# Performance work log

Hardware: AMD Instinct MI355X
Metric: run time of the kernel (lower is better)

Reference implementation:

```python
import jax, jax.numpy as jnp
import numpy as np

EPS = 1e-5  # torch GroupNorm default eps


def gn(x, g, b):
    # GroupNorm with 1 group on [N, C]: normalize over channel dim per row
    mu = jnp.mean(x, axis=-1, keepdims=True)
    var = jnp.var(x, axis=-1, keepdims=True)
    return (x - mu) * jax.lax.rsqrt(var + EPS) * g + b


def setup_inputs() -> dict:
    N, A, E, D = 500000, 20000, 500000, 128
    key = jax.random.key(0)
    ks = jax.random.split(key, 12)
    s = 0.05
    return {
        "map_x": jax.random.normal(ks[0], (N, 8), jnp.float32),
        "agt_x": jax.random.normal(ks[1], (A, 80), jnp.float32),
        "u": jax.random.randint(ks[2], (E,), 0, A),
        "v": jax.random.randint(ks[3], (E,), 0, N),
        # map_fc: Linear(8,D) with bias, then custom Linear(D,D,bias=False)+GN+ReLU
        "W0": jax.random.normal(ks[4], (D, 8), jnp.float32) * s,
        "b0": jnp.zeros((D,), jnp.float32),
        "W1": jax.random.normal(ks[5], (D, D), jnp.float32) * s,
        "g1": jnp.ones((D,), jnp.float32),
        "b1": jnp.zeros((D,), jnp.float32),
        # agt_fc: Linear(80, D, bias=False)
        "Wa": jax.random.normal(ks[6], (D, 80), jnp.float32) * s,
        # self.bn GroupNorm params
        "g_bn": jnp.ones((D,), jnp.float32),
        "b_bn": jnp.zeros((D,), jnp.float32),
        # self.fc: Linear(2D, D, bias=False)+GN+ReLU
        "Wf": jax.random.normal(ks[7], (D, 2 * D), jnp.float32) * s,
        "g_fc": jnp.ones((D,), jnp.float32),
        "b_fc": jnp.zeros((D,), jnp.float32),
    }


def reference(map_x, agt_x, u, v, W0, b0, W1, g1, b1, Wa, g_bn, b_bn, Wf, g_fc, b_fc):
    # map_fc: Linear+ReLU, then Linear(no bias)+GN+ReLU
    h = jax.nn.relu(map_x @ W0.T + b0)                      # [N, D]
    h = jax.nn.relu(gn(h @ W1.T, g1, b1))                   # [N, D]
    # agent messages: project agents once (A < E), then gather per edge
    msg = (agt_x @ Wa.T)[u]                                 # [E, D]
    tmp = jnp.zeros_like(h).at[v].add(msg)                  # scatter-add into map nodes
    tmp = jax.nn.relu(gn(tmp, g_bn, b_bn))                  # [N, D]
    cat = jnp.concatenate([h, tmp], axis=-1)                # [N, 2D]
    out = jax.nn.relu(gn(cat @ Wf.T, g_fc, b_fc))           # [N, D]
    return out
```

## Files before the change

### kernel.cpp

```cpp
#include <hip/hip_runtime.h>
#include <stdint.h>

#define EPS 1e-5f

typedef short bh8 __attribute__((ext_vector_type(8)));
typedef float f4v __attribute__((ext_vector_type(4)));
typedef unsigned short ushort_t;

static __device__ __forceinline__ unsigned short f2bf(float f) {
    unsigned u = __builtin_bit_cast(unsigned, f);
    u += 0x7fffu + ((u >> 16) & 1u);
    return (unsigned short)(u >> 16);
}

static __device__ __forceinline__ float bfbits(unsigned x) {
    return __builtin_bit_cast(float, x);
}

static __device__ __forceinline__ void acc16(float* tv, uint4 qa, uint4 qb) {
    unsigned wd[8] = {qa.x, qa.y, qa.z, qa.w, qb.x, qb.y, qb.z, qb.w};
#pragma unroll
    for (int p = 0; p < 8; ++p) {
        tv[2 * p + 0] += bfbits(wd[p] << 16);
        tv[2 * p + 1] += bfbits(wd[p] & 0xffff0000u);
    }
}


__global__ void prep(const float* __restrict__ W1, const float* __restrict__ Wf,
                     const float* __restrict__ Wa, ushort_t* __restrict__ W1b,
                     ushort_t* __restrict__ Wfb, float* __restrict__ WaT) {
    int i = blockIdx.x * 256 + threadIdx.x;
    if (i < 16384) W1b[i] = f2bf(W1[i]);
    else if (i < 49152) { int j = i - 16384; Wfb[j] = f2bf(Wf[j]); }
    else if (i < 59392) { int l2 = i - 49152; int k = l2 >> 7, c = l2 & 127; WaT[l2] = Wa[c * 80 + k]; }
}

__global__ __launch_bounds__(256) void proj_agents(const float* __restrict__ agt,
                                                   const float* __restrict__ WaT,
                                                   unsigned short* __restrict__ Pb) {
    __shared__ float WT[80 * 128];
    __shared__ float xT[80][32];
    int t = threadIdx.x;
    int row0 = blockIdx.x * 32;
#pragma unroll
    for (int m = 0; m < 40; ++m) WT[t + 256 * m] = WaT[t + 256 * m];
#pragma unroll
    for (int m = 0; m < 10; ++m) {
        int f = t + 256 * m;
        int r = f / 80, k = f - r * 80;
        xT[k][r] = agt[(size_t)(row0 + r) * 80 + k];
    }
    __syncthreads();
    int tx = t & 31, ty = t >> 5;
    float acc[4][4] = {};
    for (int k = 0; k < 80; ++k) {
        float4 xv = *(const float4*)&xT[k][ty * 4];
        float4 wv = *(const float4*)&WT[k * 128 + tx * 4];
        float xa[4] = {xv.x, xv.y, xv.z, xv.w};
        float wa[4] = {wv.x, wv.y, wv.z, wv.w};
#pragma unroll
        for (int i = 0; i < 4; ++i)
#pragma unroll
            for (int j = 0; j < 4; ++j) acc[i][j] = fmaf(xa[i], wa[j], acc[i][j]);
    }
#pragma unroll
    for (int i = 0; i < 4; ++i) {
        int r = row0 + ty * 4 + i;
        union { unsigned short s[4]; uint2 q; } o;
#pragma unroll
        for (int j = 0; j < 4; ++j) o.s[j] = f2bf(acc[i][j]);
        *(uint2*)&Pb[(size_t)r * 128 + tx * 4] = o.q;
    }
}

__global__ void hist_v(const int* __restrict__ v, int* __restrict__ cnt, int E) {
    int e = blockIdx.x * 256 + threadIdx.x;
    if (e < E) atomicAdd(&cnt[v[e]], 1);
}

__global__ __launch_bounds__(256) void scan1(const int* __restrict__ cnt,
                                             int* __restrict__ rp,
                                             int* __restrict__ partials, int n) {
    __shared__ int lds[256];
    int b = blockIdx.x, t = threadIdx.x;
    int base = b * 4096 + t * 16;
    int vv[16];
    int run = 0;
#pragma unroll
    for (int i = 0; i < 16; ++i) {
        int c = (base + i < n) ? cnt[base + i] : 0;
        vv[i] = run;
        run += c;
    }
    lds[t] = run;
    __syncthreads();
#pragma unroll
    for (int off = 1; off < 256; off <<= 1) {
        int x = (t >= off) ? lds[t - off] : 0;
        __syncthreads();
        lds[t] += x;
        __syncthreads();
    }
    int excl = lds[t] - run;
    if (t == 255) partials[b] = lds[255];
#pragma unroll
    for (int i = 0; i < 16; ++i)
        if (base + i < n) rp[base + i] = excl + vv[i];
}

__global__ __launch_bounds__(256) void scan2(int* __restrict__ partials, int nb) {
    __shared__ int lds[256];
    int t = threadIdx.x;
    int vv = (t < nb) ? partials[t] : 0;
    lds[t] = vv;
    __syncthreads();
#pragma unroll
    for (int off = 1; off < 256; off <<= 1) {
        int x = (t >= off) ? lds[t - off] : 0;
        __syncthreads();
        lds[t] += x;
        __syncthreads();
    }
    if (t < nb) partials[t] = lds[t] - vv;
}

__global__ void scan3(int* __restrict__ rp, const int* __restrict__ partials,
                      int n, int E) {
    int i = blockIdx.x * 256 + threadIdx.x;
    if (i < n) rp[i] += partials[i >> 12];
    if (i == 0) rp[n] = E;
}

__global__ void fill_csr(const int* __restrict__ u, const int* __restrict__ v,
                         const int* __restrict__ rp, int* __restrict__ cursor,
                         int* __restrict__ col, int E) {
    int e = blockIdx.x * 256 + threadIdx.x;
    if (e < E) {
        int vv = v[e];
        int pos = rp[vv] + atomicAdd(&cursor[vv], 1);
        col[pos] = u[e];
    }
}

__global__ __launch_bounds__(256) void gather_gn(
    const unsigned short* __restrict__ Pb, const int* __restrict__ rp,
    const int* __restrict__ col, const float* __restrict__ g_bn,
    const float* __restrict__ b_bn, ushort_t* __restrict__ catB) {
    const int t = threadIdx.x;
    const int node = blockIdx.x * 32 + (t >> 3);
    const int c0 = (t & 7) * 16;
    const int beg = rp[node];
    const int deg = rp[node + 1] - beg;
    const int ca = col[(deg > 0) ? beg : 0];
    const int cb = col[(deg > 1) ? beg + 1 : 0];
    const int cc = col[(deg > 2) ? beg + 2 : 0];
    const int cd = col[(deg > 3) ? beg + 3 : 0];
    const unsigned short* pB = Pb + c0;
    float tv[16] = {};
    if (deg > 0) { const uint4* p = (const uint4*)(pB + (size_t)ca * 128); acc16(tv, p[0], p[1]); }
    if (deg > 1) { const uint4* p = (const uint4*)(pB + (size_t)cb * 128); acc16(tv, p[0], p[1]); }
    if (deg > 2) { const uint4* p = (const uint4*)(pB + (size_t)cc * 128); acc16(tv, p[0], p[1]); }
    if (deg > 3) { const uint4* p = (const uint4*)(pB + (size_t)cd * 128); acc16(tv, p[0], p[1]); }
    for (int k = 4; k < deg; ++k) {
        const uint4* p = (const uint4*)(pB + (size_t)col[beg + k] * 128);
        acc16(tv, p[0], p[1]);
    }
    float a = 0.f, q = 0.f;
#pragma unroll
    for (int i = 0; i < 16; ++i) { a += tv[i]; q += tv[i] * tv[i]; }
#pragma unroll
    for (int msk = 1; msk < 8; msk <<= 1) {
        a += __shfl_xor(a, msk, 64);
        q += __shfl_xor(q, msk, 64);
    }
    const float mean = a * (1.f / 128.f);
    const float var = q * (1.f / 128.f) - mean * mean;
    const float inv = rsqrtf(var + EPS);
    union { unsigned short s[16]; uint4 q4[2]; } o;
#pragma unroll
    for (int i = 0; i < 16; ++i) {
        const int cch = c0 + i;
        o.s[i] = f2bf(fmaxf((tv[i] - mean) * inv * g_bn[cch] + b_bn[cch], 0.f));
    }
    uint4* dst = (uint4*)(catB + (size_t)node * 128 + c0);
    dst[0] = o.q4[0];
    dst[1] = o.q4[1];
}

__global__ __launch_bounds__(512, 4) void fused(
    const float* __restrict__ mapx, const float* __restrict__ W0,
    const float* __restrict__ b0, const ushort_t* __restrict__ W1b,
    const float* __restrict__ g1, const float* __restrict__ b1,
    const ushort_t* __restrict__ catB, const ushort_t* __restrict__ Wfb,
    const float* __restrict__ g_fc, const float* __restrict__ b_fc,
    float* __restrict__ out, int ntiles)
{
    __shared__ __align__(16) short h0s[32 * 128];
    __shared__ __align__(16) short cats[32 * 256];
    __shared__ float W0s[128 * 8];
    __shared__ float b0s[128];
    __shared__ float2 part[8][32];
    __shared__ float gA[128], bA[128], gC[128], bC[128];

    const int t = threadIdx.x;
    const int w = t >> 6;
    const int l = t & 63;
    const int l15 = l & 15, lg = l >> 4;

    if (t < 128) {
        gA[t] = g1[t];   bA[t] = b1[t];
        gC[t] = g_fc[t]; bC[t] = b_fc[t];
        b0s[t] = b0[t];
    }
    for (int i = t; i < 1024; i += 512) W0s[i] = W0[i];

    bh8 w1b[4], wfb[8];
    {
        const int wr = 16 * w + l15;
#pragma unroll
        for (int s = 0; s < 4; ++s)
            w1b[s] = *(const bh8*)(W1b + (size_t)wr * 128 + s * 32 + lg * 8);
#pragma unroll
        for (int s = 0; s < 8; ++s)
            wfb[s] = *(const bh8*)(Wfb + (size_t)wr * 256 + s * 32 + lg * 8);
    }
    __syncthreads();

    const f4v fzero = {0.f, 0.f, 0.f, 0.f};
    const int stride = (int)gridDim.x;

    for (int tile = blockIdx.x; tile < ntiles; tile += stride) {
        const int row0 = tile * 32;

        {
            const int r = t & 31, cg = t >> 5;
            float mx[8];
            const float* p = mapx + (size_t)(row0 + r) * 8;
            *(float4*)&mx[0] = *(const float4*)p;
            *(float4*)&mx[4] = *(const float4*)(p + 4);
            __align__(16) unsigned short hb[8];
#pragma unroll
            for (int c = 0; c < 8; ++c) {
                const int cc = 8 * cg + c;
                float a = b0s[cc];
#pragma unroll
                for (int j = 0; j < 8; ++j) a = fmaf(mx[j], W0s[cc * 8 + j], a);
                hb[c] = f2bf(fmaxf(a, 0.f));
            }
            const int a = (r * 256 + cg * 16) ^ ((r & 7) << 4);
            *(uint4*)((char*)h0s + a) = *(const uint4*)&hb[0];
        }
        {
            const int r2 = t >> 4, cb = (t & 15) * 8;
            uint4 q = *(const uint4*)(catB + (size_t)(row0 + r2) * 128 + cb);
            const int ad = (r2 * 512 + 256 + cb * 2) ^ ((r2 & 7) << 4);
            *(uint4*)((char*)cats + ad) = q;
        }
        __syncthreads();

        f4v acc2[2];
        acc2[0] = fzero; acc2[1] = fzero;
#pragma unroll
        for (int s = 0; s < 4; ++s) {
            bh8 af[2];
#pragma unroll
            for (int m = 0; m < 2; ++m) {
                const int row = 16 * m + l15;
                const int a = (row * 256 + s * 64 + lg * 16) ^ ((row & 7) << 4);
                af[m] = *(const bh8*)((const char*)h0s + a);
            }
#pragma unroll
            for (int m = 0; m < 2; ++m)
                acc2[m] = __builtin_amdgcn_mfma_f32_16x16x32_bf16(
                    w1b[s], af[m], acc2[m], 0, 0, 0);
        }

#pragma unroll
        for (int m = 0; m < 2; ++m) {
            float a = acc2[m][0] + acc2[m][1] + acc2[m][2] + acc2[m][3];
            float q = acc2[m][0] * acc2[m][0] + acc2[m][1] * acc2[m][1] +
                      acc2[m][2] * acc2[m][2] + acc2[m][3] * acc2[m][3];
            a += __shfl_xor(a, 16, 64); q += __shfl_xor(q, 16, 64);
            a += __shfl_xor(a, 32, 64); q += __shfl_xor(q, 32, 64);
            if (lg == 0) part[w][16 * m + l15] = make_float2(a, q);
        }
        __syncthreads();

#pragma unroll
        for (int m = 0; m < 2; ++m) {
            const int row = 16 * m + l15;
            float a = 0.f, q = 0.f;
#pragma unroll
            for (int pw = 0; pw < 8; ++pw) {
                float2 pq = part[pw][row];
                a += pq.x; q += pq.y;
            }
            const float mean = a * (1.f / 128.f);
            const float var = q * (1.f / 128.f) - mean * mean;
            const float inv = rsqrtf(var + EPS);
            const int c00 = 16 * w + 4 * lg;
            union { unsigned short s[4]; uint2 q2; } o;
#pragma unroll
            for (int reg = 0; reg < 4; ++reg) {
                float v2 = (acc2[m][reg] - mean) * inv * gA[c00 + reg] + bA[c00 + reg];
                o.s[reg] = f2bf(fmaxf(v2, 0.f));
            }
            const int ad = (row * 512 + c00 * 2) ^ ((row & 7) << 4);
            *(uint2*)((char*)cats + ad) = o.q2;
        }
        __syncthreads();

        f4v acc3[2];
        acc3[0] = fzero; acc3[1] = fzero;
#pragma unroll
        for (int s = 0; s < 8; ++s) {
            bh8 af[2];
#pragma unroll
            for (int m = 0; m < 2; ++m) {
                const int row = 16 * m + l15;
                const int a = (row * 512 + s * 64 + lg * 16) ^ ((row & 7) << 4);
                af[m] = *(const bh8*)((const char*)cats + a);
            }
#pragma unroll
            for (int m = 0; m < 2; ++m)
                acc3[m] = __builtin_amdgcn_mfma_f32_16x16x32_bf16(
                    wfb[s], af[m], acc3[m], 0, 0, 0);
        }

#pragma unroll
        for (int m = 0; m < 2; ++m) {
            float a = acc3[m][0] + acc3[m][1] + acc3[m][2] + acc3[m][3];
            float q = acc3[m][0] * acc3[m][0] + acc3[m][1] * acc3[m][1] +
                      acc3[m][2] * acc3[m][2] + acc3[m][3] * acc3[m][3];
            a += __shfl_xor(a, 16, 64); q += __shfl_xor(q, 16, 64);
            a += __shfl_xor(a, 32, 64); q += __shfl_xor(q, 32, 64);
            if (lg == 0) part[w][16 * m + l15] = make_float2(a, q);
        }
        __syncthreads();

#pragma unroll
        for (int m = 0; m < 2; ++m) {
            const int row = 16 * m + l15;
            float a = 0.f, q = 0.f;
#pragma unroll
            for (int pw = 0; pw < 8; ++pw) {
                float2 pq = part[pw][row];
                a += pq.x; q += pq.y;
            }
            const float mean = a * (1.f / 128.f);
            const float var = q * (1.f / 128.f) - mean * mean;
            const float inv = rsqrtf(var + EPS);
            const int c00 = 16 * w + 4 * lg;
            float4 o;
            o.x = fmaxf((acc3[m][0] - mean) * inv * gC[c00 + 0] + bC[c00 + 0], 0.f);
            o.y = fmaxf((acc3[m][1] - mean) * inv * gC[c00 + 1] + bC[c00 + 1], 0.f);
            o.z = fmaxf((acc3[m][2] - mean) * inv * gC[c00 + 2] + bC[c00 + 2], 0.f);
            o.w = fmaxf((acc3[m][3] - mean) * inv * gC[c00 + 3] + bC[c00 + 3], 0.f);
            *(float4*)&out[(size_t)(row0 + row) * 128 + c00] = o;
        }
        __syncthreads();
    }
}

extern "C" void kernel_launch(void* const* d_in, const int* in_sizes, int n_in,
                              void* d_out, int out_size, void* d_ws, size_t ws_size,
                              hipStream_t stream) {
    const float* mapx = (const float*)d_in[0];
    const float* agt  = (const float*)d_in[1];
    const int*   u    = (const int*)d_in[2];
    const int*   v    = (const int*)d_in[3];
    const float* W0   = (const float*)d_in[4];
    const float* b0   = (const float*)d_in[5];
    const float* W1   = (const float*)d_in[6];
    const float* g1   = (const float*)d_in[7];
    const float* b1   = (const float*)d_in[8];
    const float* Wa   = (const float*)d_in[9];
    const float* g_bn = (const float*)d_in[10];
    const float* b_bn = (const float*)d_in[11];
    const float* Wf   = (const float*)d_in[12];
    const float* g_fc = (const float*)d_in[13];
    const float* b_fc = (const float*)d_in[14];
    int N = in_sizes[0] / 8;
    int A = in_sizes[1] / 80;
    int E = in_sizes[2];
    float* out = (float*)d_out;

    char* ws = (char*)d_ws;
    unsigned short* Pb  = (unsigned short*)(ws + 0);
    float*    WaT       = (float*)(ws + 5120000);
    ushort_t* W1b       = (ushort_t*)(ws + 5160960);
    ushort_t* Wfb       = (ushort_t*)(ws + 5193728);
    int*      cnt       = (int*)(ws + 5259264);
    int*      cursor    = (int*)(ws + 7259264);
    int*      rp        = (int*)(ws + 9259264);
    int*      partials  = (int*)(ws + 11259392);
    int*      colv      = (int*)(ws + 11261440);
    ushort_t* catB      = (ushort_t*)(ws + 16777216);

    const int nb_scan = (N + 4095) / 4096;
    const int nb_e = (E + 255) / 256;

    prep<<<232, 256, 0, stream>>>(W1, Wf, Wa, W1b, Wfb, WaT);
    hipMemsetAsync(cnt, 0, 4000000, stream);
    hist_v<<<nb_e, 256, 0, stream>>>(v, cnt, E);
    proj_agents<<<A / 32, 256, 0, stream>>>(agt, WaT, Pb);
    scan1<<<nb_scan, 256, 0, stream>>>(cnt, rp, partials, N);
    scan2<<<1, 256, 0, stream>>>(partials, nb_scan);
    scan3<<<(N + 255) / 256, 256, 0, stream>>>(rp, partials, N, E);
    fill_csr<<<nb_e, 256, 0, stream>>>(u, v, rp, cursor, colv, E);
    gather_gn<<<N / 32, 256, 0, stream>>>(Pb, rp, colv, g_bn, b_bn, catB);

    int ntiles = N / 32;
    fused<<<512, 512, 0, stream>>>(mapx, W0, b0, W1b, g1, b1, catB,
                                   Wfb, g_fc, b_fc, out, ntiles);
}
```

Baseline: 385.0 us.

## Process two 32-row tiles per iteration in fused GEMM kernel

Each block iteration now handles a pair of 32-row tiles with separate LDS buffers, interleaving their MFMA chains and sharing each barrier across both tiles. This halves the number of __syncthreads per row and raises instruction-level parallelism in the MFMA and reduction phases. It also drops the trailing barrier at the end of each iteration, relying on the double buffers and the next iteration's barriers for ordering. The cost is double the LDS footprint and more live registers, which may lower occupancy under launch_bounds(512,4).

```diff
diff --git a/kernel.cpp b/kernel.cpp
--- a/kernel.cpp
+++ b/kernel.cpp
@@ -196,11 +196,11 @@
     const float* __restrict__ g_fc, const float* __restrict__ b_fc,
     float* __restrict__ out, int ntiles)
 {
-    __shared__ __align__(16) short h0s[32 * 128];
-    __shared__ __align__(16) short cats[32 * 256];
+    __shared__ __align__(16) short h0sA[32 * 128], h0sB[32 * 128];
+    __shared__ __align__(16) short catsA[32 * 256], catsB[32 * 256];
     __shared__ float W0s[128 * 8];
     __shared__ float b0s[128];
-    __shared__ float2 part[8][32];
+    __shared__ float2 partA[8][32], partB[8][32];
     __shared__ float gA[128], bA[128], gC[128], bC[128];
 
     const int t = threadIdx.x;
@@ -229,137 +229,220 @@
 
     const f4v fzero = {0.f, 0.f, 0.f, 0.f};
     const int stride = (int)gridDim.x;
-
-    for (int tile = blockIdx.x; tile < ntiles; tile += stride) {
-        const int row0 = tile * 32;
+    const int npairs = (ntiles + 1) >> 1;
+
+    for (int j = blockIdx.x; j < npairs; j += stride) {
+        const int tileA = 2 * j, tileB = 2 * j + 1;
+        const bool hasB = (tileB < ntiles);
+        const int rowA0 = tileA * 32, rowB0 = tileB * 32;
 
         {
             const int r = t & 31, cg = t >> 5;
-            float mx[8];
-            const float* p = mapx + (size_t)(row0 + r) * 8;
-            *(float4*)&mx[0] = *(const float4*)p;
-            *(float4*)&mx[4] = *(const float4*)(p + 4);
-            __align__(16) unsigned short hb[8];
-#pragma unroll
-            for (int c = 0; c < 8; ++c) {
-                const int cc = 8 * cg + c;
-                float a = b0s[cc];
-#pragma unroll
-                for (int j = 0; j < 8; ++j) a = fmaf(mx[j], W0s[cc * 8 + j], a);
-                hb[c] = f2bf(fmaxf(a, 0.f));
-            }
-            const int a = (r * 256 + cg * 16) ^ ((r & 7) << 4);
-            *(uint4*)((char*)h0s + a) = *(const uint4*)&hb[0];
+            const int ad = (r * 256 + cg * 16) ^ ((r & 7) << 4);
+            {
+                float mx[8];
+                const float* p = mapx + (size_t)(rowA0 + r) * 8;
+                *(float4*)&mx[0] = *(const float4*)p;
+                *(float4*)&mx[4] = *(const float4*)(p + 4);
+                __align__(16) unsigned short hb[8];
+#pragma unroll
+                for (int c = 0; c < 8; ++c) {
+                    const int cc = 8 * cg + c;
+                    float a = b0s[cc];
+#pragma unroll
+                    for (int jj = 0; jj < 8; ++jj) a = fmaf(mx[jj], W0s[cc * 8 + jj], a);
+                    hb[c] = f2bf(fmaxf(a, 0.f));
+                }
+                *(uint4*)((char*)h0sA + ad) = *(const uint4*)&hb[0];
+            }
+            if (hasB) {
+                float mx[8];
+                const float* p = mapx + (size_t)(rowB0 + r) * 8;
+                *(float4*)&mx[0] = *(const float4*)p;
+                *(float4*)&mx[4] = *(const float4*)(p + 4);
+                __align__(16) unsigned short hb[8];
+#pragma unroll
+                for (int c = 0; c < 8; ++c) {
+                    const int cc = 8 * cg + c;
+                    float a = b0s[cc];
+#pragma unroll
+                    for (int jj = 0; jj < 8; ++jj) a = fmaf(mx[jj], W0s[cc * 8 + jj], a);
+                    hb[c] = f2bf(fmaxf(a, 0.f));
+                }
+                *(uint4*)((char*)h0sB + ad) = *(const uint4*)&hb[0];
+            }
         }
         {
             const int r2 = t >> 4, cb = (t & 15) * 8;
-            uint4 q = *(const uint4*)(catB + (size_t)(row0 + r2) * 128 + cb);
             const int ad = (r2 * 512 + 256 + cb * 2) ^ ((r2 & 7) << 4);
-            *(uint4*)((char*)cats + ad) = q;
-        }
-        __syncthreads();
-
-        f4v acc2[2];
-        acc2[0] = fzero; acc2[1] = fzero;
+            uint4 qa = *(const uint4*)(catB + (size_t)(rowA0 + r2) * 128 + cb);
+            *(uint4*)((char*)catsA + ad) = qa;
+            if (hasB) {
+                uint4 qb = *(const uint4*)(catB + (size_t)(rowB0 + r2) * 128 + cb);
+                *(uint4*)((char*)catsB + ad) = qb;
+            }
+        }
+        __syncthreads();
+
+        f4v a2A[2], a2B[2];
+        a2A[0] = fzero; a2A[1] = fzero; a2B[0] = fzero; a2B[1] = fzero;
 #pragma unroll
         for (int s = 0; s < 4; ++s) {
-            bh8 af[2];
+            bh8 afA[2], afB[2];
 #pragma unroll
             for (int m = 0; m < 2; ++m) {
                 const int row = 16 * m + l15;
                 const int a = (row * 256 + s * 64 + lg * 16) ^ ((row & 7) << 4);
-                af[m] = *(const bh8*)((const char*)h0s + a);
-            }
-#pragma unroll
-            for (int m = 0; m < 2; ++m)
-                acc2[m] = __builtin_amdgcn_mfma_f32_16x16x32_bf16(
-                    w1b[s], af[m], acc2[m], 0, 0, 0);
+                afA[m] = *(const bh8*)((const char*)h0sA + a);
+                afB[m] = *(const bh8*)((const char*)h0sB + a);
+            }
+#pragma unroll
+            for (int m = 0; m < 2; ++m) {
+                a2A[m] = __builtin_amdgcn_mfma_f32_16x16x32_bf16(w1b[s], afA[m], a2A[m], 0, 0, 0);
+                a2B[m] = __builtin_amdgcn_mfma_f32_16x16x32_bf16(w1b[s], afB[m], a2B[m], 0, 0, 0);
+            }
         }
 
 #pragma unroll
         for (int m = 0; m < 2; ++m) {
-            float a = acc2[m][0] + acc2[m][1] + acc2[m][2] + acc2[m][3];
-            float q = acc2[m][0] * acc2[m][0] + acc2[m][1] * acc2[m][1] +
-                      acc2[m][2] * acc2[m][2] + acc2[m][3] * acc2[m][3];
-            a += __shfl_xor(a, 16, 64); q += __shfl_xor(q, 16, 64);
-            a += __shfl_xor(a, 32, 64); q += __shfl_xor(q, 32, 64);
-            if (lg == 0) part[w][16 * m + l15] = make_float2(a, q);
+            float aA = a2A[m][0] + a2A[m][1] + a2A[m][2] + a2A[m][3];
+            float qA = a2A[m][0] * a2A[m][0] + a2A[m][1] * a2A[m][1] +
+                       a2A[m][2] * a2A[m][2] + a2A[m][3] * a2A[m][3];
+            float aB = a2B[m][0] + a2B[m][1] + a2B[m][2] + a2B[m][3];
+            float qB = a2B[m][0] * a2B[m][0] + a2B[m][1] * a2B[m][1] +
+                       a2B[m][2] * a2B[m][2] + a2B[m][3] * a2B[m][3];
+            aA += __shfl_xor(aA, 16, 64); qA += __shfl_xor(qA, 16, 64);
+            aA += __shfl_xor(aA, 32, 64); qA += __shfl_xor(qA, 32, 64);
+            aB += __shfl_xor(aB, 16, 64); qB += __shfl_xor(qB, 16, 64);
+            aB += __shfl_xor(aB, 32, 64); qB += __shfl_xor(qB, 32, 64);
+            if (lg == 0) {
+                partA[w][16 * m + l15] = make_float2(aA, qA);
+                partB[w][16 * m + l15] = make_float2(aB, qB);
+            }
         }
         __syncthreads();
 
 #pragma unroll
         for (int m = 0; m < 2; ++m) {
             const int row = 16 * m + l15;
-            float a = 0.f, q = 0.f;
-#pragma unroll
-            for (int pw = 0; pw < 8; ++pw) {
-                float2 pq = part[pw][row];
-                a += pq.x; q += pq.y;
-            }
-            const float mean = a * (1.f / 128.f);
-            const float var = q * (1.f / 128.f) - mean * mean;
-            const float inv = rsqrtf(var + EPS);
             const int c00 = 16 * w + 4 * lg;
-            union { unsigned short s[4]; uint2 q2; } o;
-#pragma unroll
-            for (int reg = 0; reg < 4; ++reg) {
-                float v2 = (acc2[m][reg] - mean) * inv * gA[c00 + reg] + bA[c00 + reg];
-                o.s[reg] = f2bf(fmaxf(v2, 0.f));
-            }
             const int ad = (row * 512 + c00 * 2) ^ ((row & 7) << 4);
-            *(uint2*)((char*)cats + ad) = o.q2;
-        }
-        __syncthreads();
-
-        f4v acc3[2];
-        acc3[0] = fzero; acc3[1] = fzero;
+            {
+                float a = 0.f, q = 0.f;
+#pragma unroll
+                for (int pw = 0; pw < 8; ++pw) {
+                    float2 pq = partA[pw][row];
+                    a += pq.x; q += pq.y;
+                }
+                const float mean = a * (1.f / 128.f);
+                const float var = q * (1.f / 128.f) - mean * mean;
+                const float inv = rsqrtf(var + EPS);
+                union { unsigned short s[4]; uint2 q2; } o;
+#pragma unroll
+                for (int reg = 0; reg < 4; ++reg) {
+                    float v2 = (a2A[m][reg] - mean) * inv * gA[c00 + reg] + bA[c00 + reg];
+                    o.s[reg] = f2bf(fmaxf(v2, 0.f));
+                }
+                *(uint2*)((char*)catsA + ad) = o.q2;
+            }
+            {
+                float a = 0.f, q = 0.f;
+#pragma unroll
+                for (int pw = 0; pw < 8; ++pw) {
+                    float2 pq = partB[pw][row];
+                    a += pq.x; q += pq.y;
+                }
+                const float mean = a * (1.f / 128.f);
+                const float var = q * (1.f / 128.f) - mean * mean;
+                const float inv = rsqrtf(var + EPS);
+                union { unsigned short s[4]; uint2 q2; } o;
+#pragma unroll
+                for (int reg = 0; reg < 4; ++reg) {
+                    float v2 = (a2B[m][reg] - mean) * inv * gA[c00 + reg] + bA[c00 + reg];
+                    o.s[reg] = f2bf(fmaxf(v2, 0.f));
+                }
+                *(uint2*)((char*)catsB + ad) = o.q2;
+            }
+        }
+        __syncthreads();
+
+        f4v a3A[2], a3B[2];
+        a3A[0] = fzero; a3A[1] = fzero; a3B[0] = fzero; a3B[1] = fzero;
 #pragma unroll
         for (int s = 0; s < 8; ++s) {
-            bh8 af[2];
+            bh8 afA[2], afB[2];
 #pragma unroll
             for (int m = 0; m < 2; ++m) {
                 const int row = 16 * m + l15;
                 const int a = (row * 512 + s * 64 + lg * 16) ^ ((row & 7) << 4);
-                af[m] = *(const bh8*)((const char*)cats + a);
-            }
-#pragma unroll
-            for (int m = 0; m < 2; ++m)
-                acc3[m] = __builtin_amdgcn_mfma_f32_16x16x32_bf16(
-                    wfb[s], af[m], acc3[m], 0, 0, 0);
+                afA[m] = *(const bh8*)((const char*)catsA + a);
+                afB[m] = *(const bh8*)((const char*)catsB + a);
+            }
+#pragma unroll
+            for (int m = 0; m < 2; ++m) {
+                a3A[m] = __builtin_amdgcn_mfma_f32_16x16x32_bf16(wfb[s], afA[m], a3A[m], 0, 0, 0);
+                a3B[m] = __builtin_amdgcn_mfma_f32_16x16x32_bf16(wfb[s], afB[m], a3B[m], 0, 0, 0);
+            }
         }
 
 #pragma unroll
         for (int m = 0; m < 2; ++m) {
-            float a = acc3[m][0] + acc3[m][1] + acc3[m][2] + acc3[m][3];
-            float q = acc3[m][0] * acc3[m][0] + acc3[m][1] * acc3[m][1] +
-                      acc3[m][2] * acc3[m][2] + acc3[m][3] * acc3[m][3];
-            a += __shfl_xor(a, 16, 64); q += __shfl_xor(q, 16, 64);
-            a += __shfl_xor(a, 32, 64); q += __shfl_xor(q, 32, 64);
-            if (lg == 0) part[w][16 * m + l15] = make_float2(a, q);
+            float aA = a3A[m][0] + a3A[m][1] + a3A[m][2] + a3A[m][3];
+            float qA = a3A[m][0] * a3A[m][0] + a3A[m][1] * a3A[m][1] +
+                       a3A[m][2] * a3A[m][2] + a3A[m][3] * a3A[m][3];
+            float aB = a3B[m][0] + a3B[m][1] + a3B[m][2] + a3B[m][3];
+            float qB = a3B[m][0] * a3B[m][0] + a3B[m][1] * a3B[m][1] +
+                       a3B[m][2] * a3B[m][2] + a3B[m][3] * a3B[m][3];
+            aA += __shfl_xor(aA, 16, 64); qA += __shfl_xor(qA, 16, 64);
+            aA += __shfl_xor(aA, 32, 64); qA += __shfl_xor(qA, 32, 64);
+            aB += __shfl_xor(aB, 16, 64); qB += __shfl_xor(qB, 16, 64);
+            aB += __shfl_xor(aB, 32, 64); qB += __shfl_xor(qB, 32, 64);
+            if (lg == 0) {
+                partA[w][16 * m + l15] = make_float2(aA, qA);
+                partB[w][16 * m + l15] = make_float2(aB, qB);
+            }
         }
         __syncthreads();
 
 #pragma unroll
         for (int m = 0; m < 2; ++m) {
             const int row = 16 * m + l15;
-            float a = 0.f, q = 0.f;
-#pragma unroll
-            for (int pw = 0; pw < 8; ++pw) {
-                float2 pq = part[pw][row];
-                a += pq.x; q += pq.y;
-            }
-            const float mean = a * (1.f / 128.f);
-            const float var = q * (1.f / 128.f) - mean * mean;
-            const float inv = rsqrtf(var + EPS);
             const int c00 = 16 * w + 4 * lg;
-            float4 o;
-            o.x = fmaxf((acc3[m][0] - mean) * inv * gC[c00 + 0] + bC[c00 + 0], 0.f);
-            o.y = fmaxf((acc3[m][1] - mean) * inv * gC[c00 + 1] + bC[c00 + 1], 0.f);
-            o.z = fmaxf((acc3[m][2] - mean) * inv * gC[c00 + 2] + bC[c00 + 2], 0.f);
-            o.w = fmaxf((acc3[m][3] - mean) * inv * gC[c00 + 3] + bC[c00 + 3], 0.f);
-            *(float4*)&out[(size_t)(row0 + row) * 128 + c00] = o;
-        }
-        __syncthreads();
+            {
+                float a = 0.f, q = 0.f;
+#pragma unroll
+                for (int pw = 0; pw < 8; ++pw) {
+                    float2 pq = partA[pw][row];
+                    a += pq.x; q += pq.y;
+                }
+                const float mean = a * (1.f / 128.f);
+                const float var = q * (1.f / 128.f) - mean * mean;
+                const float inv = rsqrtf(var + EPS);
+                float4 o;
+                o.x = fmaxf((a3A[m][0] - mean) * inv * gC[c00 + 0] + bC[c00 + 0], 0.f);
+                o.y = fmaxf((a3A[m][1] - mean) * inv * gC[c00 + 1] + bC[c00 + 1], 0.f);
+                o.z = fmaxf((a3A[m][2] - mean) * inv * gC[c00 + 2] + bC[c00 + 2], 0.f);
+                o.w = fmaxf((a3A[m][3] - mean) * inv * gC[c00 + 3] + bC[c00 + 3], 0.f);
+                *(float4*)&out[(size_t)(rowA0 + row) * 128 + c00] = o;
+            }
+            if (hasB) {
+                float a = 0.f, q = 0.f;
+#pragma unroll
+                for (int pw = 0; pw < 8; ++pw) {
+                    float2 pq = partB[pw][row];
+                    a += pq.x; q += pq.y;
+                }
+                const float mean = a * (1.f / 128.f);
+                const float var = q * (1.f / 128.f) - mean * mean;
+                const float inv = rsqrtf(var + EPS);
+                float4 o;
+                o.x = fmaxf((a3B[m][0] - mean) * inv * gC[c00 + 0] + bC[c00 + 0], 0.f);
+                o.y = fmaxf((a3B[m][1] - mean) * inv * gC[c00 + 1] + bC[c00 + 1], 0.f);
+                o.z = fmaxf((a3B[m][2] - mean) * inv * gC[c00 + 2] + bC[c00 + 2], 0.f);
+                o.w = fmaxf((a3B[m][3] - mean) * inv * gC[c00 + 3] + bC[c00 + 3], 0.f);
+                *(float4*)&out[(size_t)(rowB0 + row) * 128 + c00] = o;
+            }
+        }
     }
 }
 
```

Result: faster. 349.1 us (-9.3%).

## Process two row tiles per block iteration with 32-column warp slices

Applied to the files above, without the earlier changes.

Each block iteration now handles two 32-row tiles. Warps are split into two groups of four, one group per tile, and each warp covers 32 output columns (two 16-wide MFMA n-blocks) instead of 16. Each A fragment loaded from LDS is therefore reused across two MFMAs. The per-warp partial stats array is replaced by LDS atomicAdd into per-tile row sums, and the trailing barrier is dropped. The cost is twice the LDS buffers and twice the weight registers, which may lower occupancy.

```diff
diff --git a/kernel.cpp b/kernel.cpp
--- a/kernel.cpp
+++ b/kernel.cpp
@@ -196,17 +196,19 @@
     const float* __restrict__ g_fc, const float* __restrict__ b_fc,
     float* __restrict__ out, int ntiles)
 {
-    __shared__ __align__(16) short h0s[32 * 128];
-    __shared__ __align__(16) short cats[32 * 256];
+    __shared__ __align__(16) short h0sA[32 * 128], h0sB[32 * 128];
+    __shared__ __align__(16) short catsA[32 * 256], catsB[32 * 256];
     __shared__ float W0s[128 * 8];
     __shared__ float b0s[128];
-    __shared__ float2 part[8][32];
+    __shared__ float S2[2][32], Q2[2][32], S3[2][32], Q3[2][32];
     __shared__ float gA[128], bA[128], gC[128], bC[128];
 
     const int t = threadIdx.x;
     const int w = t >> 6;
     const int l = t & 63;
     const int l15 = l & 15, lg = l >> 4;
+    const int tw = w >> 2;
+    const int cbase = 32 * (w & 3);
 
     if (t < 128) {
         gA[t] = g1[t];   bA[t] = b1[t];
@@ -215,151 +217,204 @@
     }
     for (int i = t; i < 1024; i += 512) W0s[i] = W0[i];
 
-    bh8 w1b[4], wfb[8];
-    {
-        const int wr = 16 * w + l15;
+    bh8 w1b[2][4], wfb[2][8];
+#pragma unroll
+    for (int n = 0; n < 2; ++n) {
+        const int wr = cbase + 16 * n + l15;
 #pragma unroll
         for (int s = 0; s < 4; ++s)
-            w1b[s] = *(const bh8*)(W1b + (size_t)wr * 128 + s * 32 + lg * 8);
+            w1b[n][s] = *(const bh8*)(W1b + (size_t)wr * 128 + s * 32 + lg * 8);
 #pragma unroll
         for (int s = 0; s < 8; ++s)
-            wfb[s] = *(const bh8*)(Wfb + (size_t)wr * 256 + s * 32 + lg * 8);
+            wfb[n][s] = *(const bh8*)(Wfb + (size_t)wr * 256 + s * 32 + lg * 8);
     }
     __syncthreads();
 
     const f4v fzero = {0.f, 0.f, 0.f, 0.f};
     const int stride = (int)gridDim.x;
-
-    for (int tile = blockIdx.x; tile < ntiles; tile += stride) {
-        const int row0 = tile * 32;
-
+    const int npairs = (ntiles + 1) >> 1;
+
+    for (int j = blockIdx.x; j < npairs; j += stride) {
+        const int tileA = 2 * j, tileB = 2 * j + 1;
+        const bool hasB = (tileB < ntiles);
+        const int rowA0 = tileA * 32, rowB0 = tileB * 32;
+        const bool active = (tw == 0) || hasB;
+        const int myrow0 = tw ? rowB0 : rowA0;
+        const short* h0p = tw ? h0sB : h0sA;
+        short* catsp = tw ? catsB : catsA;
+
+        if (t < 64) { ((float*)S2)[t] = 0.f; ((float*)Q2)[t] = 0.f; }
         {
             const int r = t & 31, cg = t >> 5;
-            float mx[8];
-            const float* p = mapx + (size_t)(row0 + r) * 8;
-            *(float4*)&mx[0] = *(const float4*)p;
-            *(float4*)&mx[4] = *(const float4*)(p + 4);
-            __align__(16) unsigned short hb[8];
-#pragma unroll
-            for (int c = 0; c < 8; ++c) {
-                const int cc = 8 * cg + c;
-                float a = b0s[cc];
-#pragma unroll
-                for (int j = 0; j < 8; ++j) a = fmaf(mx[j], W0s[cc * 8 + j], a);
-                hb[c] = f2bf(fmaxf(a, 0.f));
-            }
-            const int a = (r * 256 + cg * 16) ^ ((r & 7) << 4);
-            *(uint4*)((char*)h0s + a) = *(const uint4*)&hb[0];
+            const int ad = (r * 256 + cg * 16) ^ ((r & 7) << 4);
+            {
+                float mx[8];
+                const float* p = mapx + (size_t)(rowA0 + r) * 8;
+                *(float4*)&mx[0] = *(const float4*)p;
+                *(float4*)&mx[4] = *(const float4*)(p + 4);
+                __align__(16) unsigned short hb[8];
+#pragma unroll
+                for (int c = 0; c < 8; ++c) {
+                    const int cc = 8 * cg + c;
+                    float a = b0s[cc];
+#pragma unroll
+                    for (int jj = 0; jj < 8; ++jj) a = fmaf(mx[jj], W0s[cc * 8 + jj], a);
+                    hb[c] = f2bf(fmaxf(a, 0.f));
+                }
+                *(uint4*)((char*)h0sA + ad) = *(const uint4*)&hb[0];
+            }
+            if (hasB) {
+                float mx[8];
+                const float* p = mapx + (size_t)(rowB0 + r) * 8;
+                *(float4*)&mx[0] = *(const float4*)p;
+                *(float4*)&mx[4] = *(const float4*)(p + 4);
+                __align__(16) unsigned short hb[8];
+#pragma unroll
+                for (int c = 0; c < 8; ++c) {
+                    const int cc = 8 * cg + c;
+                    float a = b0s[cc];
+#pragma unroll
+                    for (int jj = 0; jj < 8; ++jj) a = fmaf(mx[jj], W0s[cc * 8 + jj], a);
+                    hb[c] = f2bf(fmaxf(a, 0.f));
+                }
+                *(uint4*)((char*)h0sB + ad) = *(const uint4*)&hb[0];
+            }
         }
         {
             const int r2 = t >> 4, cb = (t & 15) * 8;
-            uint4 q = *(const uint4*)(catB + (size_t)(row0 + r2) * 128 + cb);
             const int ad = (r2 * 512 + 256 + cb * 2) ^ ((r2 & 7) << 4);
-            *(uint4*)((char*)cats + ad) = q;
-        }
-        __syncthreads();
-
-        f4v acc2[2];
-        acc2[0] = fzero; acc2[1] = fzero;
-#pragma unroll
-        for (int s = 0; s < 4; ++s) {
-            bh8 af[2];
+            uint4 qa = *(const uint4*)(catB + (size_t)(rowA0 + r2) * 128 + cb);
+            *(uint4*)((char*)catsA + ad) = qa;
+            if (hasB) {
+                uint4 qb = *(const uint4*)(catB + (size_t)(rowB0 + r2) * 128 + cb);
+                *(uint4*)((char*)catsB + ad) = qb;
+            }
+        }
+        __syncthreads();
+
+        if (t < 64) { ((float*)S3)[t] = 0.f; ((float*)Q3)[t] = 0.f; }
+        f4v acc2[2][2];
+        acc2[0][0] = fzero; acc2[0][1] = fzero; acc2[1][0] = fzero; acc2[1][1] = fzero;
+        if (active) {
+#pragma unroll
+            for (int s = 0; s < 4; ++s) {
+                bh8 af[2];
+#pragma unroll
+                for (int m = 0; m < 2; ++m) {
+                    const int row = 16 * m + l15;
+                    const int a = (row * 256 + s * 64 + lg * 16) ^ ((row & 7) << 4);
+                    af[m] = *(const bh8*)((const char*)h0p + a);
+                }
+#pragma unroll
+                for (int m = 0; m < 2; ++m)
+#pragma unroll
+                    for (int n = 0; n < 2; ++n)
+                        acc2[m][n] = __builtin_amdgcn_mfma_f32_16x16x32_bf16(
+                            w1b[n][s], af[m], acc2[m][n], 0, 0, 0);
+            }
+#pragma unroll
+            for (int m = 0; m < 2; ++m) {
+                float a = 0.f, q = 0.f;
+#pragma unroll
+                for (int n = 0; n < 2; ++n)
+#pragma unroll
+                    for (int reg = 0; reg < 4; ++reg) {
+                        float x = acc2[m][n][reg];
+                        a += x; q += x * x;
+                    }
+                a += __shfl_xor(a, 16, 64); q += __shfl_xor(q, 16, 64);
+                a += __shfl_xor(a, 32, 64); q += __shfl_xor(q, 32, 64);
+                if (lg == 0) {
+                    atomicAdd(&S2[tw][16 * m + l15], a);
+                    atomicAdd(&Q2[tw][16 * m + l15], q);
+                }
+            }
+        }
+        __syncthreads();
+
+        if (active) {
 #pragma unroll
             for (int m = 0; m < 2; ++m) {
                 const int row = 16 * m + l15;
-                const int a = (row * 256 + s * 64 + lg * 16) ^ ((row & 7) << 4);
-                af[m] = *(const bh8*)((const char*)h0s + a);
-            }
-#pragma unroll
-            for (int m = 0; m < 2; ++m)
-                acc2[m] = __builtin_amdgcn_mfma_f32_16x16x32_bf16(
-                    w1b[s], af[m], acc2[m], 0, 0, 0);
-        }
-
-#pragma unroll
-        for (int m = 0; m < 2; ++m) {
-            float a = acc2[m][0] + acc2[m][1] + acc2[m][2] + acc2[m][3];
-            float q = acc2[m][0] * acc2[m][0] + acc2[m][1] * acc2[m][1] +
-                      acc2[m][2] * acc2[m][2] + acc2[m][3] * acc2[m][3];
-            a += __shfl_xor(a, 16, 64); q += __shfl_xor(q, 16, 64);
-            a += __shfl_xor(a, 32, 64); q += __shfl_xor(q, 32, 64);
-            if (lg == 0) part[w][16 * m + l15] = make_float2(a, q);
-        }
-        __syncthreads();
-
-#pragma unroll
-        for (int m = 0; m < 2; ++m) {
-            const int row = 16 * m + l15;
-            float a = 0.f, q = 0.f;
-#pragma unroll
-            for (int pw = 0; pw < 8; ++pw) {
-                float2 pq = part[pw][row];
-                a += pq.x; q += pq.y;
-            }
-            const float mean = a * (1.f / 128.f);
-            const float var = q * (1.f / 128.f) - mean * mean;
-            const float inv = rsqrtf(var + EPS);
-            const int c00 = 16 * w + 4 * lg;
-            union { unsigned short s[4]; uint2 q2; } o;
-#pragma unroll
-            for (int reg = 0; reg < 4; ++reg) {
-                float v2 = (acc2[m][reg] - mean) * inv * gA[c00 + reg] + bA[c00 + reg];
-                o.s[reg] = f2bf(fmaxf(v2, 0.f));
-            }
-            const int ad = (row * 512 + c00 * 2) ^ ((row & 7) << 4);
-            *(uint2*)((char*)cats + ad) = o.q2;
-        }
-        __syncthreads();
-
-        f4v acc3[2];
-        acc3[0] = fzero; acc3[1] = fzero;
-#pragma unroll
-        for (int s = 0; s < 8; ++s) {
-            bh8 af[2];
+                const float a = S2[tw][row], q = Q2[tw][row];
+                const float mean = a * (1.f / 128.f);
+                const float var = q * (1.f / 128.f) - mean * mean;
+                const float inv = rsqrtf(var + EPS);
+#pragma unroll
+                for (int n = 0; n < 2; ++n) {
+                    const int c00 = cbase + 16 * n + 4 * lg;
+                    union { unsigned short s[4]; uint2 q2; } o;
+#pragma unroll
+                    for (int reg = 0; reg < 4; ++reg) {
+                        float v2 = (acc2[m][n][reg] - mean) * inv * gA[c00 + reg] + bA[c00 + reg];
+                        o.s[reg] = f2bf(fmaxf(v2, 0.f));
+                    }
+                    const int ad = (row * 512 + c00 * 2) ^ ((row & 7) << 4);
+                    *(uint2*)((char*)catsp + ad) = o.q2;
+                }
+            }
+        }
+        __syncthreads();
+
+        f4v acc3[2][2];
+        acc3[0][0] = fzero; acc3[0][1] = fzero; acc3[1][0] = fzero; acc3[1][1] = fzero;
+        if (active) {
+#pragma unroll
+            for (int s = 0; s < 8; ++s) {
+                bh8 af[2];
+#pragma unroll
+                for (int m = 0; m < 2; ++m) {
+                    const int row = 16 * m + l15;
+                    const int a = (row * 512 + s * 64 + lg * 16) ^ ((row & 7) << 4);
+                    af[m] = *(const bh8*)((const char*)catsp + a);
+                }
+#pragma unroll
+                for (int m = 0; m < 2; ++m)
+#pragma unroll
+                    for (int n = 0; n < 2; ++n)
+                        acc3[m][n] = __builtin_amdgcn_mfma_f32_16x16x32_bf16(
+                            wfb[n][s], af[m], acc3[m][n], 0, 0, 0);
+            }
+#pragma unroll
+            for (int m = 0; m < 2; ++m) {
+                float a = 0.f, q = 0.f;
+#pragma unroll
+                for (int n = 0; n < 2; ++n)
+#pragma unroll
+                    for (int reg = 0; reg < 4; ++reg) {
+                        float x = acc3[m][n][reg];
+                        a += x; q += x * x;
+                    }
+                a += __shfl_xor(a, 16, 64); q += __shfl_xor(q, 16, 64);
+                a += __shfl_xor(a, 32, 64); q += __shfl_xor(q, 32, 64);
+                if (lg == 0) {
+                    atomicAdd(&S3[tw][16 * m + l15], a);
+                    atomicAdd(&Q3[tw][16 * m + l15], q);
+                }
+            }
+        }
+        __syncthreads();
+
+        if (active) {
 #pragma unroll
             for (int m = 0; m < 2; ++m) {
                 const int row = 16 * m + l15;
-                const int a = (row * 512 + s * 64 + lg * 16) ^ ((row & 7) << 4);
-                af[m] = *(const bh8*)((const char*)cats + a);
-            }
-#pragma unroll
-            for (int m = 0; m < 2; ++m)
-                acc3[m] = __builtin_amdgcn_mfma_f32_16x16x32_bf16(
-                    wfb[s], af[m], acc3[m], 0, 0, 0);
-        }
-
-#pragma unroll
-        for (int m = 0; m < 2; ++m) {
-            float a = acc3[m][0] + acc3[m][1] + acc3[m][2] + acc3[m][3];
-            float q = acc3[m][0] * acc3[m][0] + acc3[m][1] * acc3[m][1] +
-                      acc3[m][2] * acc3[m][2] + acc3[m][3] * acc3[m][3];
-            a += __shfl_xor(a, 16, 64); q += __shfl_xor(q, 16, 64);
-            a += __shfl_xor(a, 32, 64); q += __shfl_xor(q, 32, 64);
-            if (lg == 0) part[w][16 * m + l15] = make_float2(a, q);
-        }
-        __syncthreads();
-
-#pragma unroll
-        for (int m = 0; m < 2; ++m) {
-            const int row = 16 * m + l15;
-            float a = 0.f, q = 0.f;
-#pragma unroll
-            for (int pw = 0; pw < 8; ++pw) {
-                float2 pq = part[pw][row];
-                a += pq.x; q += pq.y;
-            }
-            const float mean = a * (1.f / 128.f);
-            const float var = q * (1.f / 128.f) - mean * mean;
-            const float inv = rsqrtf(var + EPS);
-            const int c00 = 16 * w + 4 * lg;
-            float4 o;
-            o.x = fmaxf((acc3[m][0] - mean) * inv * gC[c00 + 0] + bC[c00 + 0], 0.f);
-            o.y = fmaxf((acc3[m][1] - mean) * inv * gC[c00 + 1] + bC[c00 + 1], 0.f);
-            o.z = fmaxf((acc3[m][2] - mean) * inv * gC[c00 + 2] + bC[c00 + 2], 0.f);
-            o.w = fmaxf((acc3[m][3] - mean) * inv * gC[c00 + 3] + bC[c00 + 3], 0.f);
-            *(float4*)&out[(size_t)(row0 + row) * 128 + c00] = o;
-        }
-        __syncthreads();
+                const float a = S3[tw][row], q = Q3[tw][row];
+                const float mean = a * (1.f / 128.f);
+                const float var = q * (1.f / 128.f) - mean * mean;
+                const float inv = rsqrtf(var + EPS);
+#pragma unroll
+                for (int n = 0; n < 2; ++n) {
+                    const int c00 = cbase + 16 * n + 4 * lg;
+                    float4 o;
+                    o.x = fmaxf((acc3[m][n][0] - mean) * inv * gC[c00 + 0] + bC[c00 + 0], 0.f);
+                    o.y = fmaxf((acc3[m][n][1] - mean) * inv * gC[c00 + 1] + bC[c00 + 1], 0.f);
+                    o.z = fmaxf((acc3[m][n][2] - mean) * inv * gC[c00 + 2] + bC[c00 + 2], 0.f);
+                    o.w = fmaxf((acc3[m][n][3] - mean) * inv * gC[c00 + 3] + bC[c00 + 3], 0.f);
+                    *(float4*)&out[(size_t)(myrow0 + row) * 128 + c00] = o;
+                }
+            }
+        }
     }
 }
 
```

Measured after the change: 462.5 us. 1.2x slower.
